# Kernel tuning notes

Measured on AMD Instinct MI355X. Metric: run time of the kernel, lower is better.

Reference implementation:

```python
import jax, jax.numpy as jnp
import numpy as np

B, DIM, COND, HID = 500000, 3, 64, 128
IN = DIM + COND + 1  # z + context + time feature


def setup_inputs() -> dict:
    key = jax.random.key(0)
    ks = jax.random.split(key, 8)
    s_in = 1.0 / np.sqrt(IN)
    s_h = 1.0 / np.sqrt(HID)
    return {
        "t": jnp.float32(0.5),
        "z": jax.random.normal(ks[0], (B, DIM), jnp.float32),
        "logp": jnp.zeros((B, 1), jnp.float32),
        "context": jax.random.normal(ks[1], (B, COND), jnp.float32),
        "eps": jax.random.normal(ks[2], (B, DIM), jnp.float32),
        "W_in": jax.random.normal(ks[3], (IN, HID), jnp.float32) * s_in,
        "b_in": jnp.zeros((HID,), jnp.float32),
        "W_h1": jax.random.normal(ks[4], (HID, HID), jnp.float32) * s_h,
        "b_h1": jnp.zeros((HID,), jnp.float32),
        "W_h2": jax.random.normal(ks[5], (HID, HID), jnp.float32) * s_h,
        "b_h2": jnp.zeros((HID,), jnp.float32),
        "W_out": jax.random.normal(ks[6], (HID, DIM), jnp.float32) * s_h,
        "b_out": jnp.zeros((DIM,), jnp.float32),
        "out_scale": jnp.float32(1.0),
    }


def reference(t, z, logp, context, eps, W_in, b_in, W_h1, b_h1, W_h2, b_h2,
              W_out, b_out, out_scale):
    t_feat = jnp.full((z.shape[0], 1), t, dtype=z.dtype)

    def vel(zz):
        inp = jnp.concatenate([zz, context, t_feat], axis=1)  # (B, IN)
        h = jnp.tanh(inp @ W_in + b_in)
        h = jnp.tanh(h @ W_h1 + b_h1)
        h = jnp.tanh(h @ W_h2 + b_h2)
        return (h @ W_out + b_out) * out_scale  # (B, DIM)

    # Hutchinson trace: tr(df/dz) ~= eps^T (d/dz)(f . eps) via vjp with cotangent eps
    f, vjp_fn = jax.vjp(vel, z)
    (gz,) = vjp_fn(eps)
    neg_div = -jnp.sum(gz * eps, axis=1, keepdims=True)  # (B, 1)
    return f, neg_div
```

## Files before the change

kernel.cpp:

```cpp
#include <hip/hip_runtime.h>


#define B_N    500000
#define NT32   15625
#define GRID   256
#define WPB    12
#define NSTR   (GRID * WPB)

#define L_WFIN   0
#define L_WF1    8704
#define L_WF2    25600
#define L_WB2    42496
#define L_WB1    59392
#define L_WOUTP  76288
#define L_WOUTT  76800
#define L_WIN3   77196
#define L_F16END 77592
#define N_BIAS   384
#define PREP_N   (L_F16END + N_BIAS)
#define BIAS_BYTE   155184
#define OUTST_BYTE  156720
#define LDS_BYTES   161328
#define COPY16      9795

typedef _Float16 f16x4 __attribute__((ext_vector_type(4)));
typedef _Float16 f16x8 __attribute__((ext_vector_type(8)));
typedef float    f32x4 __attribute__((ext_vector_type(4)));

union U4 { f16x4 v; _Float16 e[4]; uint2 d; };
union U8 { f16x8 v; f16x4 h[2]; _Float16 e[8]; uint2 d2[2]; };

static __device__ inline f16x4 lds_a4(const _Float16* p) {
    U4 u; u.d = *reinterpret_cast<const uint2*>(p); return u.v;
}
static __device__ inline f16x8 lds_a8(const _Float16* p) {
    U8 u;
    u.d2[0] = *reinterpret_cast<const uint2*>(p);
    u.d2[1] = *reinterpret_cast<const uint2*>(p + 4);
    return u.v;
}

#define MFMA16(a, b, c) __builtin_amdgcn_mfma_f32_16x16x16f16((a), (b), (c), 0, 0, 0)
#define MFMA32(a, b, c) __builtin_amdgcn_mfma_f32_16x16x32_f16((a), (b), (c), 0, 0, 0)

static __device__ inline float ftanh(float x) {
    float e = __expf(2.f * x);
    return 1.f - 2.f * __builtin_amdgcn_rcpf(e + 1.f);
}

static __device__ inline int sig(int p) {
    return (p & ~31) | ((p & 4) << 2) | ((p >> 1) & 12) | (p & 3);
}

__global__ void prep_kernel(const float* __restrict__ W_in,
                            const float* __restrict__ W_h1,
                            const float* __restrict__ W_h2,
                            const float* __restrict__ W_out,
                            const float* __restrict__ b_in,
                            const float* __restrict__ b_h1,
                            const float* __restrict__ b_h2,
                            _Float16* __restrict__ ws) {
    int i = blockIdx.x * 256 + threadIdx.x;
    if (i >= PREP_N) return;
    if (i >= L_F16END) {
        int bi = i - L_F16END;
        float* bp = reinterpret_cast<float*>(ws + L_F16END);
        bp[bi] = (bi < 128) ? b_in[bi] : (bi < 256) ? b_h1[bi - 128]
                                                    : b_h2[bi - 256];
        return;
    }
    float v = 0.f;
    if (i < L_WF1) {
        int n = i / 68, k = i - n * 68;
        if      (k < 64)  v = W_in[(3 + k) * 128 + n];
        else if (k < 67)  v = W_in[(k - 64) * 128 + n];
        else              v = W_in[67 * 128 + n];
    } else if (i < L_WF2) {
        int j = i - L_WF1; int n = j / 132, a = j - n * 132;
        if (a < 128) v = W_h1[sig(a) * 128 + n];
    } else if (i < L_WB2) {
        int j = i - L_WF2; int n = j / 132, a = j - n * 132;
        if (a < 128) v = W_h2[sig(a) * 128 + n];
    } else if (i < L_WB1) {
        int j = i - L_WB2; int r = j / 132, b = j - r * 132;
        if (b < 128) v = W_h2[r * 128 + sig(b)];
    } else if (i < L_WOUTP) {
        int j = i - L_WB1; int r = j / 132, b = j - r * 132;
        if (b < 128) v = W_h1[r * 128 + sig(b)];
    } else if (i < L_WOUTT) {
        int j = i - L_WOUTP; int n = j >> 2, k = j & 3;
        if (k < 3) v = W_out[n * 3 + k];
    } else if (i < L_WIN3) {
        int j = i - L_WOUTT; int d = j / 132, n = j - d * 132;
        if (n < 128) v = W_out[sig(n) * 3 + d];
    } else {
        int j = i - L_WIN3; int d = j / 132, a = j - d * 132;
        if (a < 128) v = W_in[d * 128 + sig(a)];
    }
    ws[i] = (_Float16)v;
}

__global__ __launch_bounds__(768, 3) void fused_kernel(
        const float* __restrict__ t_p,  const float* __restrict__ z,
        const float* __restrict__ ctx,  const float* __restrict__ eps,
        const float* __restrict__ b_out, const float* __restrict__ os_p,
        const _Float16* __restrict__ ws, float* __restrict__ out) {
    extern __shared__ _Float16 smem[];
    const int tid  = threadIdx.x;
    const int wave = tid >> 6;
    const int lane = tid & 63;
    const int l15  = lane & 15;
    const int q    = lane >> 4;

    {
        const uint4* src = reinterpret_cast<const uint4*>(ws);
        uint4* dst = reinterpret_cast<uint4*>(smem);
        for (int i = tid; i < COPY16; i += 768) dst[i] = src[i];
    }
    __syncthreads();

    const _Float16* WFIN  = smem + L_WFIN;
    const _Float16* WF1   = smem + L_WF1;
    const _Float16* WF2   = smem + L_WF2;
    const _Float16* WB2   = smem + L_WB2;
    const _Float16* WB1   = smem + L_WB1;
    const _Float16* WOUTP = smem + L_WOUTP;
    const _Float16* WOUTT = smem + L_WOUTT;
    const _Float16* WIN3  = smem + L_WIN3;
    const float* biasf =
        reinterpret_cast<const float*>(reinterpret_cast<char*>(smem) + BIAS_BYTE);
    float* outst =
        reinterpret_cast<float*>(reinterpret_cast<char*>(smem) + OUTST_BYTE)
        + wave * 96;

    const float tval = t_p[0];
    const float os   = os_p[0];
    const float bo0 = b_out[0], bo1 = b_out[1], bo2 = b_out[2];
    float* out_f  = out;
    float* out_nd = out + (size_t)B_N * 3;

    const f32x4 zero4 = {0.f, 0.f, 0.f, 0.f};

    for (int t = blockIdx.x + wave * GRID; t < NT32; t += NSTR) {
        const int gb = t * 32;

        U4 epsb[2];
        float ee[2][3];
        #pragma unroll
        for (int c = 0; c < 2; ++c) {
            epsb[c].d.x = 0u; epsb[c].d.y = 0u;
            ee[c][0] = ee[c][1] = ee[c][2] = 0.f;
            if (q == 0) {
                const float* ep = eps + (size_t)(gb + 16 * c + l15) * 3;
                ee[c][0] = ep[0]; ee[c][1] = ep[1]; ee[c][2] = ep[2];
                epsb[c].e[0] = (_Float16)ee[c][0];
                epsb[c].e[1] = (_Float16)ee[c][1];
                epsb[c].e[2] = (_Float16)ee[c][2];
            }
        }

        U8 cb[2][2];
        #pragma unroll
        for (int a = 0; a < 2; ++a)
            #pragma unroll
            for (int c = 0; c < 2; ++c) {
                const float* cp = ctx + (size_t)(gb + 16 * c + l15) * 64
                                  + a * 32 + 8 * q;
                const float4 v0 = *reinterpret_cast<const float4*>(cp);
                const float4 v1 = *reinterpret_cast<const float4*>(cp + 4);
                cb[a][c].e[0] = (_Float16)v0.x; cb[a][c].e[1] = (_Float16)v0.y;
                cb[a][c].e[2] = (_Float16)v0.z; cb[a][c].e[3] = (_Float16)v0.w;
                cb[a][c].e[4] = (_Float16)v1.x; cb[a][c].e[5] = (_Float16)v1.y;
                cb[a][c].e[6] = (_Float16)v1.z; cb[a][c].e[7] = (_Float16)v1.w;
            }
        U4 bz[2];
        #pragma unroll
        for (int c = 0; c < 2; ++c) {
            bz[c].d.x = 0u; bz[c].d.y = 0u;
            if (q == 0) {
                const float* zp = z + (size_t)(gb + 16 * c + l15) * 3;
                bz[c].e[0] = (_Float16)zp[0]; bz[c].e[1] = (_Float16)zp[1];
                bz[c].e[2] = (_Float16)zp[2]; bz[c].e[3] = (_Float16)tval;
            }
        }

        U8 h1p[4][2];
        #pragma unroll
        for (int m = 0; m < 8; ++m) {
            f32x4 a0 = zero4, a1 = zero4;
            #pragma unroll
            for (int a = 0; a < 2; ++a) {
                f16x8 A = lds_a8(WFIN + (16 * m + l15) * 68 + a * 32 + 8 * q);
                a0 = MFMA32(A, cb[a][0].v, a0);
                a1 = MFMA32(A, cb[a][1].v, a1);
            }
            {
                f16x4 A4 = lds_a4(WFIN + (16 * m + l15) * 68 + 64 + 4 * q);
                a0 = MFMA16(A4, bz[0].v, a0);
                a1 = MFMA16(A4, bz[1].v, a1);
            }
            const float4 bb = *reinterpret_cast<const float4*>(
                biasf + 0 + 16 * m + 4 * q);
            #pragma unroll
            for (int c = 0; c < 2; ++c) {
                const f32x4 ac = c ? a1 : a0;
                h1p[m >> 1][c].e[(m & 1) * 4 + 0] = (_Float16)ftanh(ac[0] + bb.x);
                h1p[m >> 1][c].e[(m & 1) * 4 + 1] = (_Float16)ftanh(ac[1] + bb.y);
                h1p[m >> 1][c].e[(m & 1) * 4 + 2] = (_Float16)ftanh(ac[2] + bb.z);
                h1p[m >> 1][c].e[(m & 1) * 4 + 3] = (_Float16)ftanh(ac[3] + bb.w);
            }
        }

        U8 h2p[4][2];
        #pragma unroll
        for (int m = 0; m < 8; ++m) {
            f32x4 a0 = zero4, a1 = zero4;
            #pragma unroll
            for (int a = 0; a < 4; ++a) {
                f16x8 A = lds_a8(WF1 + (16 * m + l15) * 132 + a * 32 + 8 * q);
                a0 = MFMA32(A, h1p[a][0].v, a0);
                a1 = MFMA32(A, h1p[a][1].v, a1);
            }
            const float4 bb = *reinterpret_cast<const float4*>(
                biasf + 128 + 16 * m + 4 * q);
            #pragma unroll
            for (int c = 0; c < 2; ++c) {
                const f32x4 ac = c ? a1 : a0;
                h2p[m >> 1][c].e[(m & 1) * 4 + 0] = (_Float16)ftanh(ac[0] + bb.x);
                h2p[m >> 1][c].e[(m & 1) * 4 + 1] = (_Float16)ftanh(ac[1] + bb.y);
                h2p[m >> 1][c].e[(m & 1) * 4 + 2] = (_Float16)ftanh(ac[2] + bb.z);
                h2p[m >> 1][c].e[(m & 1) * 4 + 3] = (_Float16)ftanh(ac[3] + bb.w);
            }
        }

        U8 u3p[4][2];
        f32x4 f0 = zero4, f1 = zero4;
        #pragma unroll
        for (int mp = 0; mp < 4; ++mp) {
            U8 h3pr[2];
            #pragma unroll
            for (int sub = 0; sub < 2; ++sub) {
                const int m = 2 * mp + sub;
                f32x4 a0 = zero4, a1 = zero4;
                #pragma unroll
                for (int a = 0; a < 4; ++a) {
                    f16x8 A = lds_a8(WF2 + (16 * m + l15) * 132 + a * 32 + 8 * q);
                    a0 = MFMA32(A, h2p[a][0].v, a0);
                    a1 = MFMA32(A, h2p[a][1].v, a1);
                }
                f16x4 a3 = lds_a4(WOUTP + (16 * m + l15) * 4 + 4 * q);
                f32x4 up0 = MFMA16(a3, epsb[0].v, zero4);
                f32x4 up1 = MFMA16(a3, epsb[1].v, zero4);
                const float4 bb = *reinterpret_cast<const float4*>(
                    biasf + 256 + 16 * m + 4 * q);
                #pragma unroll
                for (int c = 0; c < 2; ++c) {
                    const f32x4 ac = c ? a1 : a0;
                    const f32x4 uc = c ? up1 : up0;
                    #pragma unroll
                    for (int i = 0; i < 4; ++i) {
                        float bi = (i == 0) ? bb.x : (i == 1) ? bb.y
                                  : (i == 2) ? bb.z : bb.w;
                        float h = ftanh(ac[i] + bi);
                        h3pr[c].e[sub * 4 + i] = (_Float16)h;
                        u3p[mp][c].e[sub * 4 + i] =
                            (_Float16)(os * uc[i] * (1.f - h * h));
                    }
                }
            }
            f16x8 Af = lds_a8(WOUTT + l15 * 132 + mp * 32 + 8 * q);
            f0 = MFMA32(Af, h3pr[0].v, f0);
            f1 = MFMA32(Af, h3pr[1].v, f1);
        }
        if (q == 0) {
            outst[(0 * 16 + l15) * 3 + 0] = (f0[0] + bo0) * os;
            outst[(0 * 16 + l15) * 3 + 1] = (f0[1] + bo1) * os;
            outst[(0 * 16 + l15) * 3 + 2] = (f0[2] + bo2) * os;
            outst[(1 * 16 + l15) * 3 + 0] = (f1[0] + bo0) * os;
            outst[(1 * 16 + l15) * 3 + 1] = (f1[1] + bo1) * os;
            outst[(1 * 16 + l15) * 3 + 2] = (f1[2] + bo2) * os;
        }

        #pragma unroll
        for (int m = 0; m < 8; ++m) {
            f32x4 a0 = zero4, a1 = zero4;
            #pragma unroll
            for (int a = 0; a < 4; ++a) {
                f16x8 A = lds_a8(WB2 + (16 * m + l15) * 132 + a * 32 + 8 * q);
                a0 = MFMA32(A, u3p[a][0].v, a0);
                a1 = MFMA32(A, u3p[a][1].v, a1);
            }
            #pragma unroll
            for (int c = 0; c < 2; ++c) {
                const f32x4 ac = c ? a1 : a0;
                #pragma unroll
                for (int i = 0; i < 4; ++i) {
                    float h = (float)h2p[m >> 1][c].e[(m & 1) * 4 + i];
                    h2p[m >> 1][c].e[(m & 1) * 4 + i] =
                        (_Float16)(ac[i] * (1.f - h * h));
                }
            }
        }

        f32x4 g0 = zero4, g1 = zero4;
        #pragma unroll
        for (int mp = 0; mp < 4; ++mp) {
            U8 u1pr[2];
            #pragma unroll
            for (int sub = 0; sub < 2; ++sub) {
                const int m = 2 * mp + sub;
                f32x4 a0 = zero4, a1 = zero4;
                #pragma unroll
                for (int a = 0; a < 4; ++a) {
                    f16x8 A = lds_a8(WB1 + (16 * m + l15) * 132 + a * 32 + 8 * q);
                    a0 = MFMA32(A, h2p[a][0].v, a0);
                    a1 = MFMA32(A, h2p[a][1].v, a1);
                }
                #pragma unroll
                for (int c = 0; c < 2; ++c) {
                    const f32x4 ac = c ? a1 : a0;
                    #pragma unroll
                    for (int i = 0; i < 4; ++i) {
                        float h = (float)h1p[m >> 1][c].e[(m & 1) * 4 + i];
                        u1pr[c].e[sub * 4 + i] =
                            (_Float16)(ac[i] * (1.f - h * h));
                    }
                }
            }
            f16x8 Ag = lds_a8(WIN3 + l15 * 132 + mp * 32 + 8 * q);
            g0 = MFMA32(Ag, u1pr[0].v, g0);
            g1 = MFMA32(Ag, u1pr[1].v, g1);
        }
        if (q == 0) {
            out_nd[gb + l15] =
                -(g0[0] * ee[0][0] + g0[1] * ee[0][1] + g0[2] * ee[0][2]);
            out_nd[gb + 16 + l15] =
                -(g1[0] * ee[1][0] + g1[1] * ee[1][1] + g1[2] * ee[1][2]);
        }

        if (lane < 24) {
            float4 v = *reinterpret_cast<const float4*>(outst + lane * 4);
            *reinterpret_cast<float4*>(out_f + (size_t)gb * 3 + lane * 4) = v;
        }
    }
}

extern "C" void kernel_launch(void* const* d_in, const int* in_sizes, int n_in,
                              void* d_out, int out_size, void* d_ws, size_t ws_size,
                              hipStream_t stream) {
    const float* t_p   = (const float*)d_in[0];
    const float* z     = (const float*)d_in[1];
    const float* ctx   = (const float*)d_in[3];
    const float* eps   = (const float*)d_in[4];
    const float* W_in  = (const float*)d_in[5];
    const float* b_in  = (const float*)d_in[6];
    const float* W_h1  = (const float*)d_in[7];
    const float* b_h1  = (const float*)d_in[8];
    const float* W_h2  = (const float*)d_in[9];
    const float* b_h2  = (const float*)d_in[10];
    const float* W_out = (const float*)d_in[11];
    const float* b_out = (const float*)d_in[12];
    const float* os_p  = (const float*)d_in[13];
    _Float16* ws = (_Float16*)d_ws;
    float* out = (float*)d_out;

    static bool attr_set = false;
    if (!attr_set) {
        (void)hipFuncSetAttribute((const void*)fused_kernel,
                                  hipFuncAttributeMaxDynamicSharedMemorySize,
                                  LDS_BYTES);
        attr_set = true;
    }

    prep_kernel<<<(PREP_N + 255) / 256, 256, 0, stream>>>(
        W_in, W_h1, W_h2, W_out, b_in, b_h1, b_h2, ws);
    fused_kernel<<<GRID, 768, LDS_BYTES, stream>>>(
        t_p, z, ctx, eps, b_out, os_p, ws, out);
}
```

Baseline: 356.0 us.

## Use 8 waves per block, native f16 vectors, and contiguous tile assignment

Cuts waves per block from 12 to 8 (512 threads) and relaxes launch bounds so each wave gets more registers. Replaces the union-based fp16 packing with native ext_vector types so the compiler can keep operands in registers without extra moves. Tile assignment changes to contiguous per-block ranges. Fewer waves per block reduce latency hiding but should lower register pressure and avoid spills.

```diff
diff --git a/kernel.cpp b/kernel.cpp
--- a/kernel.cpp
+++ b/kernel.cpp
@@ -4,7 +4,7 @@
 #define B_N    500000
 #define NT32   15625
 #define GRID   256
-#define WPB    12
+#define WPB    8
 #define NSTR   (GRID * WPB)
 
 #define L_WFIN   0
@@ -20,24 +20,20 @@
 #define PREP_N   (L_F16END + N_BIAS)
 #define BIAS_BYTE   155184
 #define OUTST_BYTE  156720
-#define LDS_BYTES   161328
+#define LDS_BYTES   159792
 #define COPY16      9795
 
 typedef _Float16 f16x4 __attribute__((ext_vector_type(4)));
 typedef _Float16 f16x8 __attribute__((ext_vector_type(8)));
 typedef float    f32x4 __attribute__((ext_vector_type(4)));
 
-union U4 { f16x4 v; _Float16 e[4]; uint2 d; };
-union U8 { f16x8 v; f16x4 h[2]; _Float16 e[8]; uint2 d2[2]; };
-
 static __device__ inline f16x4 lds_a4(const _Float16* p) {
-    U4 u; u.d = *reinterpret_cast<const uint2*>(p); return u.v;
+    return *reinterpret_cast<const f16x4*>(p);
 }
 static __device__ inline f16x8 lds_a8(const _Float16* p) {
-    U8 u;
-    u.d2[0] = *reinterpret_cast<const uint2*>(p);
-    u.d2[1] = *reinterpret_cast<const uint2*>(p + 4);
-    return u.v;
+    f16x4 lo = *reinterpret_cast<const f16x4*>(p);
+    f16x4 hi = *reinterpret_cast<const f16x4*>(p + 4);
+    return __builtin_shufflevector(lo, hi, 0, 1, 2, 3, 4, 5, 6, 7);
 }
 
 #define MFMA16(a, b, c) __builtin_amdgcn_mfma_f32_16x16x16f16((a), (b), (c), 0, 0, 0)
@@ -47,6 +43,12 @@
     float e = __expf(2.f * x);
     return 1.f - 2.f * __builtin_amdgcn_rcpf(e + 1.f);
 }
+
+#define TANH4(dst, sub, acv, bb)                               \
+    dst[(sub) * 4 + 0] = (_Float16)ftanh((acv)[0] + (bb).x);   \
+    dst[(sub) * 4 + 1] = (_Float16)ftanh((acv)[1] + (bb).y);   \
+    dst[(sub) * 4 + 2] = (_Float16)ftanh((acv)[2] + (bb).z);   \
+    dst[(sub) * 4 + 3] = (_Float16)ftanh((acv)[3] + (bb).w);
 
 static __device__ inline int sig(int p) {
     return (p & ~31) | ((p & 4) << 2) | ((p >> 1) & 12) | (p & 3);
@@ -100,7 +102,7 @@
     ws[i] = (_Float16)v;
 }
 
-__global__ __launch_bounds__(768, 3) void fused_kernel(
+__global__ __launch_bounds__(512, 1) void fused_kernel(
         const float* __restrict__ t_p,  const float* __restrict__ z,
         const float* __restrict__ ctx,  const float* __restrict__ eps,
         const float* __restrict__ b_out, const float* __restrict__ os_p,
@@ -115,7 +117,7 @@
     {
         const uint4* src = reinterpret_cast<const uint4*>(ws);
         uint4* dst = reinterpret_cast<uint4*>(smem);
-        for (int i = tid; i < COPY16; i += 768) dst[i] = src[i];
+        for (int i = tid; i < COPY16; i += 512) dst[i] = src[i];
     }
     __syncthreads();
 
@@ -140,26 +142,28 @@
     float* out_nd = out + (size_t)B_N * 3;
 
     const f32x4 zero4 = {0.f, 0.f, 0.f, 0.f};
-
-    for (int t = blockIdx.x + wave * GRID; t < NT32; t += NSTR) {
+    const _Float16 hz = (_Float16)0.f;
+
+    for (int t = blockIdx.x * WPB + wave; t < NT32; t += NSTR) {
         const int gb = t * 32;
 
-        U4 epsb[2];
+        f16x4 epsb[2];
         float ee[2][3];
         #pragma unroll
         for (int c = 0; c < 2; ++c) {
-            epsb[c].d.x = 0u; epsb[c].d.y = 0u;
+            f16x4 ev = {hz, hz, hz, hz};
             ee[c][0] = ee[c][1] = ee[c][2] = 0.f;
             if (q == 0) {
                 const float* ep = eps + (size_t)(gb + 16 * c + l15) * 3;
                 ee[c][0] = ep[0]; ee[c][1] = ep[1]; ee[c][2] = ep[2];
-                epsb[c].e[0] = (_Float16)ee[c][0];
-                epsb[c].e[1] = (_Float16)ee[c][1];
-                epsb[c].e[2] = (_Float16)ee[c][2];
-            }
-        }
-
-        U8 cb[2][2];
+                ev[0] = (_Float16)ee[c][0];
+                ev[1] = (_Float16)ee[c][1];
+                ev[2] = (_Float16)ee[c][2];
+            }
+            epsb[c] = ev;
+        }
+
+        f16x8 cb[2][2];
         #pragma unroll
         for (int a = 0; a < 2; ++a)
             #pragma unroll
@@ -168,76 +172,67 @@
                                   + a * 32 + 8 * q;
                 const float4 v0 = *reinterpret_cast<const float4*>(cp);
                 const float4 v1 = *reinterpret_cast<const float4*>(cp + 4);
-                cb[a][c].e[0] = (_Float16)v0.x; cb[a][c].e[1] = (_Float16)v0.y;
-                cb[a][c].e[2] = (_Float16)v0.z; cb[a][c].e[3] = (_Float16)v0.w;
-                cb[a][c].e[4] = (_Float16)v1.x; cb[a][c].e[5] = (_Float16)v1.y;
-                cb[a][c].e[6] = (_Float16)v1.z; cb[a][c].e[7] = (_Float16)v1.w;
-            }
-        U4 bz[2];
+                f16x8 cv;
+                cv[0] = (_Float16)v0.x; cv[1] = (_Float16)v0.y;
+                cv[2] = (_Float16)v0.z; cv[3] = (_Float16)v0.w;
+                cv[4] = (_Float16)v1.x; cv[5] = (_Float16)v1.y;
+                cv[6] = (_Float16)v1.z; cv[7] = (_Float16)v1.w;
+                cb[a][c] = cv;
+            }
+        f16x4 bz[2];
         #pragma unroll
         for (int c = 0; c < 2; ++c) {
-            bz[c].d.x = 0u; bz[c].d.y = 0u;
+            f16x4 zv = {hz, hz, hz, hz};
             if (q == 0) {
                 const float* zp = z + (size_t)(gb + 16 * c + l15) * 3;
-                bz[c].e[0] = (_Float16)zp[0]; bz[c].e[1] = (_Float16)zp[1];
-                bz[c].e[2] = (_Float16)zp[2]; bz[c].e[3] = (_Float16)tval;
-            }
-        }
-
-        U8 h1p[4][2];
+                zv[0] = (_Float16)zp[0]; zv[1] = (_Float16)zp[1];
+                zv[2] = (_Float16)zp[2]; zv[3] = (_Float16)tval;
+            }
+            bz[c] = zv;
+        }
+
+        f16x8 h1p[4][2];
         #pragma unroll
         for (int m = 0; m < 8; ++m) {
             f32x4 a0 = zero4, a1 = zero4;
             #pragma unroll
             for (int a = 0; a < 2; ++a) {
                 f16x8 A = lds_a8(WFIN + (16 * m + l15) * 68 + a * 32 + 8 * q);
-                a0 = MFMA32(A, cb[a][0].v, a0);
-                a1 = MFMA32(A, cb[a][1].v, a1);
+                a0 = MFMA32(A, cb[a][0], a0);
+                a1 = MFMA32(A, cb[a][1], a1);
             }
             {
                 f16x4 A4 = lds_a4(WFIN + (16 * m + l15) * 68 + 64 + 4 * q);
-                a0 = MFMA16(A4, bz[0].v, a0);
-                a1 = MFMA16(A4, bz[1].v, a1);
+                a0 = MFMA16(A4, bz[0], a0);
+                a1 = MFMA16(A4, bz[1], a1);
             }
             const float4 bb = *reinterpret_cast<const float4*>(
                 biasf + 0 + 16 * m + 4 * q);
-            #pragma unroll
-            for (int c = 0; c < 2; ++c) {
-                const f32x4 ac = c ? a1 : a0;
-                h1p[m >> 1][c].e[(m & 1) * 4 + 0] = (_Float16)ftanh(ac[0] + bb.x);
-                h1p[m >> 1][c].e[(m & 1) * 4 + 1] = (_Float16)ftanh(ac[1] + bb.y);
-                h1p[m >> 1][c].e[(m & 1) * 4 + 2] = (_Float16)ftanh(ac[2] + bb.z);
-                h1p[m >> 1][c].e[(m & 1) * 4 + 3] = (_Float16)ftanh(ac[3] + bb.w);
-            }
-        }
-
-        U8 h2p[4][2];
+            TANH4(h1p[m >> 1][0], m & 1, a0, bb);
+            TANH4(h1p[m >> 1][1], m & 1, a1, bb);
+        }
+
+        f16x8 h2p[4][2];
         #pragma unroll
         for (int m = 0; m < 8; ++m) {
             f32x4 a0 = zero4, a1 = zero4;
             #pragma unroll
             for (int a = 0; a < 4; ++a) {
                 f16x8 A = lds_a8(WF1 + (16 * m + l15) * 132 + a * 32 + 8 * q);
-                a0 = MFMA32(A, h1p[a][0].v, a0);
-                a1 = MFMA32(A, h1p[a][1].v, a1);
+                a0 = MFMA32(A, h1p[a][0], a0);
+                a1 = MFMA32(A, h1p[a][1], a1);
             }
             const float4 bb = *reinterpret_cast<const float4*>(
                 biasf + 128 + 16 * m + 4 * q);
-            #pragma unroll
-            for (int c = 0; c < 2; ++c) {
-                const f32x4 ac = c ? a1 : a0;
-                h2p[m >> 1][c].e[(m & 1) * 4 + 0] = (_Float16)ftanh(ac[0] + bb.x);
-                h2p[m >> 1][c].e[(m & 1) * 4 + 1] = (_Float16)ftanh(ac[1] + bb.y);
-                h2p[m >> 1][c].e[(m & 1) * 4 + 2] = (_Float16)ftanh(ac[2] + bb.z);
-                h2p[m >> 1][c].e[(m & 1) * 4 + 3] = (_Float16)ftanh(ac[3] + bb.w);
-            }
-        }
-
-        U8 u3p[4][2];
+            TANH4(h2p[m >> 1][0], m & 1, a0, bb);
+            TANH4(h2p[m >> 1][1], m & 1, a1, bb);
+        }
+
+        f16x8 u3p[4][2];
         f32x4 f0 = zero4, f1 = zero4;
         #pragma unroll
         for (int mp = 0; mp < 4; ++mp) {
-            U8 h3pr[2];
+            f16x8 h3p0, h3p1;
             #pragma unroll
             for (int sub = 0; sub < 2; ++sub) {
                 const int m = 2 * mp + sub;
@@ -245,32 +240,31 @@
                 #pragma unroll
                 for (int a = 0; a < 4; ++a) {
                     f16x8 A = lds_a8(WF2 + (16 * m + l15) * 132 + a * 32 + 8 * q);
-                    a0 = MFMA32(A, h2p[a][0].v, a0);
-                    a1 = MFMA32(A, h2p[a][1].v, a1);
+                    a0 = MFMA32(A, h2p[a][0], a0);
+                    a1 = MFMA32(A, h2p[a][1], a1);
                 }
                 f16x4 a3 = lds_a4(WOUTP + (16 * m + l15) * 4 + 4 * q);
-                f32x4 up0 = MFMA16(a3, epsb[0].v, zero4);
-                f32x4 up1 = MFMA16(a3, epsb[1].v, zero4);
+                f32x4 up0 = MFMA16(a3, epsb[0], zero4);
+                f32x4 up1 = MFMA16(a3, epsb[1], zero4);
                 const float4 bb = *reinterpret_cast<const float4*>(
                     biasf + 256 + 16 * m + 4 * q);
                 #pragma unroll
-                for (int c = 0; c < 2; ++c) {
-                    const f32x4 ac = c ? a1 : a0;
-                    const f32x4 uc = c ? up1 : up0;
-                    #pragma unroll
-                    for (int i = 0; i < 4; ++i) {
-                        float bi = (i == 0) ? bb.x : (i == 1) ? bb.y
-                                  : (i == 2) ? bb.z : bb.w;
-                        float h = ftanh(ac[i] + bi);
-                        h3pr[c].e[sub * 4 + i] = (_Float16)h;
-                        u3p[mp][c].e[sub * 4 + i] =
-                            (_Float16)(os * uc[i] * (1.f - h * h));
-                    }
+                for (int i = 0; i < 4; ++i) {
+                    float bi = (i == 0) ? bb.x : (i == 1) ? bb.y
+                              : (i == 2) ? bb.z : bb.w;
+                    float h0 = ftanh(a0[i] + bi);
+                    float h1v = ftanh(a1[i] + bi);
+                    h3p0[sub * 4 + i] = (_Float16)h0;
+                    h3p1[sub * 4 + i] = (_Float16)h1v;
+                    u3p[mp][0][sub * 4 + i] =
+                        (_Float16)(os * up0[i] * (1.f - h0 * h0));
+                    u3p[mp][1][sub * 4 + i] =
+                        (_Float16)(os * up1[i] * (1.f - h1v * h1v));
                 }
             }
             f16x8 Af = lds_a8(WOUTT + l15 * 132 + mp * 32 + 8 * q);
-            f0 = MFMA32(Af, h3pr[0].v, f0);
-            f1 = MFMA32(Af, h3pr[1].v, f1);
+            f0 = MFMA32(Af, h3p0, f0);
+            f1 = MFMA32(Af, h3p1, f1);
         }
         if (q == 0) {
             outst[(0 * 16 + l15) * 3 + 0] = (f0[0] + bo0) * os;
@@ -287,25 +281,24 @@
             #pragma unroll
             for (int a = 0; a < 4; ++a) {
                 f16x8 A = lds_a8(WB2 + (16 * m + l15) * 132 + a * 32 + 8 * q);
-                a0 = MFMA32(A, u3p[a][0].v, a0);
-                a1 = MFMA32(A, u3p[a][1].v, a1);
-            }
-            #pragma unroll
-            for (int c = 0; c < 2; ++c) {
-                const f32x4 ac = c ? a1 : a0;
-                #pragma unroll
-                for (int i = 0; i < 4; ++i) {
-                    float h = (float)h2p[m >> 1][c].e[(m & 1) * 4 + i];
-                    h2p[m >> 1][c].e[(m & 1) * 4 + i] =
-                        (_Float16)(ac[i] * (1.f - h * h));
-                }
+                a0 = MFMA32(A, u3p[a][0], a0);
+                a1 = MFMA32(A, u3p[a][1], a1);
+            }
+            #pragma unroll
+            for (int i = 0; i < 4; ++i) {
+                float h0 = (float)h2p[m >> 1][0][(m & 1) * 4 + i];
+                float h1v = (float)h2p[m >> 1][1][(m & 1) * 4 + i];
+                h2p[m >> 1][0][(m & 1) * 4 + i] =
+                    (_Float16)(a0[i] * (1.f - h0 * h0));
+                h2p[m >> 1][1][(m & 1) * 4 + i] =
+                    (_Float16)(a1[i] * (1.f - h1v * h1v));
             }
         }
 
         f32x4 g0 = zero4, g1 = zero4;
         #pragma unroll
         for (int mp = 0; mp < 4; ++mp) {
-            U8 u1pr[2];
+            f16x8 u1p0, u1p1;
             #pragma unroll
             for (int sub = 0; sub < 2; ++sub) {
                 const int m = 2 * mp + sub;
@@ -313,23 +306,20 @@
                 #pragma unroll
                 for (int a = 0; a < 4; ++a) {
                     f16x8 A = lds_a8(WB1 + (16 * m + l15) * 132 + a * 32 + 8 * q);
-                    a0 = MFMA32(A, h2p[a][0].v, a0);
-                    a1 = MFMA32(A, h2p[a][1].v, a1);
+                    a0 = MFMA32(A, h2p[a][0], a0);
+                    a1 = MFMA32(A, h2p[a][1], a1);
                 }
                 #pragma unroll
-                for (int c = 0; c < 2; ++c) {
-                    const f32x4 ac = c ? a1 : a0;
-                    #pragma unroll
-                    for (int i = 0; i < 4; ++i) {
-                        float h = (float)h1p[m >> 1][c].e[(m & 1) * 4 + i];
-                        u1pr[c].e[sub * 4 + i] =
-                            (_Float16)(ac[i] * (1.f - h * h));
-                    }
+                for (int i = 0; i < 4; ++i) {
+                    float h0 = (float)h1p[mp][0][sub * 4 + i];
+                    float h1v = (float)h1p[mp][1][sub * 4 + i];
+                    u1p0[sub * 4 + i] = (_Float16)(a0[i] * (1.f - h0 * h0));
+                    u1p1[sub * 4 + i] = (_Float16)(a1[i] * (1.f - h1v * h1v));
                 }
             }
             f16x8 Ag = lds_a8(WIN3 + l15 * 132 + mp * 32 + 8 * q);
-            g0 = MFMA32(Ag, u1pr[0].v, g0);
-            g1 = MFMA32(Ag, u1pr[1].v, g1);
+            g0 = MFMA32(Ag, u1p0, g0);
+            g1 = MFMA32(Ag, u1p1, g1);
         }
         if (q == 0) {
             out_nd[gb + l15] =
@@ -374,6 +364,6 @@
 
     prep_kernel<<<(PREP_N + 255) / 256, 256, 0, stream>>>(
         W_in, W_h1, W_h2, W_out, b_in, b_h1, b_h2, ws);
-    fused_kernel<<<GRID, 768, LDS_BYTES, stream>>>(
+    fused_kernel<<<GRID, 512, LDS_BYTES, stream>>>(
         t_p, z, ctx, eps, b_out, os_p, ws, out);
 }
```

New measurement: 310.4 us, median of 2. 12.8% less time.
